# Performance work log

Measured on AMD Instinct MI355X. Metric: run time of the kernel, lower is better.

## Reference

```python
import jax, jax.numpy as jnp
import numpy as np

VOXEL_RES = 4
CLASSES = 40


def setup_inputs() -> dict:
    key = jax.random.key(0)
    kx, kw, kb = jax.random.split(key, 3)
    B, N = 64, 100000
    x = jax.random.normal(kx, (B, N, 3), dtype=jnp.float32)
    F = VOXEL_RES ** 3
    bound = 1.0 / np.sqrt(F)  # torch Linear default init range
    W = jax.random.uniform(kw, (CLASSES, F), minval=-bound, maxval=bound, dtype=jnp.float32)
    b = jax.random.uniform(kb, (CLASSES,), minval=-bound, maxval=bound, dtype=jnp.float32)
    return {"x": x, "W": W, "b": b}


def reference(x, W, b):
    # x: (B, N, 3). Faithful to torch.histogramdd(bins=R): the histogram range
    # per dimension is [min, max] of the data; the last bin is right-inclusive.
    B, N, _ = x.shape
    R = VOXEL_RES
    mn = jnp.min(x, axis=1, keepdims=True)  # (B, 1, 3)
    mx = jnp.max(x, axis=1, keepdims=True)  # (B, 1, 3)
    # bin index = floor((v - min) / (max - min) * R), clipped so v == max -> R-1
    idx = jnp.floor((x - mn) / (mx - mn) * R).astype(jnp.int32)
    idx = jnp.clip(idx, 0, R - 1)  # (B, N, 3)
    flat = idx[..., 0] * R * R + idx[..., 1] * R + idx[..., 2]  # (B, N)
    flat = flat + (jnp.arange(B, dtype=jnp.int32) * (R ** 3))[:, None]
    counts = jax.ops.segment_sum(
        jnp.ones((B * N,), dtype=x.dtype), flat.reshape(-1), num_segments=B * R ** 3
    ).reshape(B, R ** 3)
    counts = counts / N  # fraction of points per voxel
    class_outputs = counts @ W.T + b  # (B, classes)
    return class_outputs
```

## Files before the change

kernel.cpp:

```cpp
#include <hip/hip_runtime.h>

#define VR 4
#define NVOX 64
#define NCLS 40
#define NB 64
#define NPTS 100000
#define BPB 16
#define NBLK (NB * BPB)
#define G_PER_B (NPTS / 4)
#define F4_PER_B (NPTS * 3 / 4)
#define STRIDE_G (BPB * 256)
#define FULL_ITERS (G_PER_B / STRIDE_G)
#define TAIL_G (G_PER_B - FULL_ITERS * STRIDE_G)
#define SW_LD 41
#define FLT_BIG 3.402823466e38f

static __device__ __forceinline__ int bin1(float v, float mn, float s4) {
    int i = (int)((v - mn) * s4);
    return i > (VR - 1) ? (VR - 1) : i;
}

static __device__ __forceinline__ unsigned long long vox_mask(
        int v, const unsigned long long* ns) {
    return (__ballot(v & 1)  ^ ns[0]) & (__ballot(v & 2)  ^ ns[1])
         & (__ballot(v & 4)  ^ ns[2]) & (__ballot(v & 8)  ^ ns[3])
         & (__ballot(v & 16) ^ ns[4]) & (__ballot(v & 32) ^ ns[5]);
}


__global__ __launch_bounds__(256) void minmax_k(const float4* __restrict__ x,
                                                float* __restrict__ pmin,
                                                float* __restrict__ pmax,
                                                float* __restrict__ out) {
    const int bid = blockIdx.x;
    const int b = bid & (NB - 1);
    const int sub = bid >> 6;
    const float4* xb = x + (size_t)b * F4_PER_B;
    const int lane = threadIdx.x & 63;
    const int wv = threadIdx.x >> 6;
    const int t0 = sub * 256 + (int)threadIdx.x;

    if (sub == 0 && threadIdx.x < NCLS)
        out[b * NCLS + threadIdx.x] = 0.f;

    float mn0 = FLT_BIG, mn1 = FLT_BIG, mn2 = FLT_BIG;
    float mx0 = -FLT_BIG, mx1 = -FLT_BIG, mx2 = -FLT_BIG;
    #pragma unroll
    for (int k = 0; k < FULL_ITERS; k++) {
        const int g = t0 + k * STRIDE_G;
        const float4 a = xb[3 * g], c = xb[3 * g + 1], e = xb[3 * g + 2];
        mn0 = fminf(mn0, fminf(fminf(a.x, a.w), fminf(c.z, e.y)));
        mx0 = fmaxf(mx0, fmaxf(fmaxf(a.x, a.w), fmaxf(c.z, e.y)));
        mn1 = fminf(mn1, fminf(fminf(a.y, c.x), fminf(c.w, e.z)));
        mx1 = fmaxf(mx1, fmaxf(fmaxf(a.y, c.x), fmaxf(c.w, e.z)));
        mn2 = fminf(mn2, fminf(fminf(a.z, c.y), fminf(e.x, e.w)));
        mx2 = fmaxf(mx2, fmaxf(fmaxf(a.z, c.y), fmaxf(e.x, e.w)));
    }
    if (sub * 256 < TAIL_G && t0 < TAIL_G) {
        const int g = FULL_ITERS * STRIDE_G + t0;
        const float4 a = xb[3 * g], c = xb[3 * g + 1], e = xb[3 * g + 2];
        mn0 = fminf(mn0, fminf(fminf(a.x, a.w), fminf(c.z, e.y)));
        mx0 = fmaxf(mx0, fmaxf(fmaxf(a.x, a.w), fmaxf(c.z, e.y)));
        mn1 = fminf(mn1, fminf(fminf(a.y, c.x), fminf(c.w, e.z)));
        mx1 = fmaxf(mx1, fmaxf(fmaxf(a.y, c.x), fmaxf(c.w, e.z)));
        mn2 = fminf(mn2, fminf(fminf(a.z, c.y), fminf(e.x, e.w)));
        mx2 = fmaxf(mx2, fmaxf(fmaxf(a.z, c.y), fmaxf(e.x, e.w)));
    }

    #pragma unroll
    for (int off = 32; off > 0; off >>= 1) {
        mn0 = fminf(mn0, __shfl_down(mn0, off, 64));
        mn1 = fminf(mn1, __shfl_down(mn1, off, 64));
        mn2 = fminf(mn2, __shfl_down(mn2, off, 64));
        mx0 = fmaxf(mx0, __shfl_down(mx0, off, 64));
        mx1 = fmaxf(mx1, __shfl_down(mx1, off, 64));
        mx2 = fmaxf(mx2, __shfl_down(mx2, off, 64));
    }

    __shared__ float smn[4][3], smx[4][3];
    if (lane == 0) {
        smn[wv][0] = mn0; smn[wv][1] = mn1; smn[wv][2] = mn2;
        smx[wv][0] = mx0; smx[wv][1] = mx1; smx[wv][2] = mx2;
    }
    __syncthreads();
    if (threadIdx.x < 3) {
        const int d = threadIdx.x;
        float a = smn[0][d], z = smx[0][d];
        #pragma unroll
        for (int w = 1; w < 4; w++) {
            a = fminf(a, smn[w][d]);
            z = fmaxf(z, smx[w][d]);
        }
        pmin[(b * BPB + sub) * 3 + d] = a;
        pmax[(b * BPB + sub) * 3 + d] = z;
    }
}

__global__ __launch_bounds__(256) void hist_gemv_k(const float4* __restrict__ x,
                                                   const float* __restrict__ pmin,
                                                   const float* __restrict__ pmax,
                                                   const float* __restrict__ W,
                                                   const float* __restrict__ bias,
                                                   float* __restrict__ out) {
    const int bid = blockIdx.x;
    const int b = bid & (NB - 1);
    const int sub = bid >> 6;
    const float4* xb = x + (size_t)b * F4_PER_B;
    const int lane = threadIdx.x & 63;
    const int wv = threadIdx.x >> 6;
    const int t0 = sub * 256 + (int)threadIdx.x;

    __shared__ float sW[NVOX * SW_LD];
    __shared__ float smm[6];
    __shared__ unsigned swh[4][NVOX];
    __shared__ float fh[NVOX];

    for (int i = threadIdx.x; i < NCLS * NVOX; i += 256)
        sW[(i % NVOX) * SW_LD + (i / NVOX)] = W[i];

    if (threadIdx.x < 6) {
        const int d = threadIdx.x % 3;
        const bool isMax = threadIdx.x >= 3;
        float r = isMax ? -FLT_BIG : FLT_BIG;
        for (int s = 0; s < BPB; s++) {
            float v = isMax ? pmax[(b * BPB + s) * 3 + d]
                            : pmin[(b * BPB + s) * 3 + d];
            r = isMax ? fmaxf(r, v) : fminf(r, v);
        }
        smm[threadIdx.x] = r;
    }
    __syncthreads();
    const float bn0 = smm[0], bn1 = smm[1], bn2 = smm[2];
    const float s40 = (float)VR / (smm[3] - smm[0]);
    const float s41 = (float)VR / (smm[4] - smm[1]);
    const float s42 = (float)VR / (smm[5] - smm[2]);

    unsigned long long ns[6];
    #pragma unroll
    for (int k = 0; k < 6; k++)
        ns[k] = ((lane >> k) & 1) ? 0ull : ~0ull;

    unsigned cnt = 0;
    if (sub * 256 < TAIL_G) {
        const bool valid = t0 < TAIL_G;
        const unsigned long long vm = __ballot(valid);
        const int g = FULL_ITERS * STRIDE_G + (valid ? t0 : 0);
        const float4 a = xb[3 * g], c = xb[3 * g + 1], e = xb[3 * g + 2];
        int v0 = bin1(a.x, bn0, s40) * 16 + bin1(a.y, bn1, s41) * 4 + bin1(a.z, bn2, s42);
        int v1 = bin1(a.w, bn0, s40) * 16 + bin1(c.x, bn1, s41) * 4 + bin1(c.y, bn2, s42);
        int v2 = bin1(c.z, bn0, s40) * 16 + bin1(c.w, bn1, s41) * 4 + bin1(e.x, bn2, s42);
        int v3 = bin1(e.y, bn0, s40) * 16 + bin1(e.z, bn1, s41) * 4 + bin1(e.w, bn2, s42);
        cnt += (unsigned)__popcll(vm & vox_mask(v0, ns));
        cnt += (unsigned)__popcll(vm & vox_mask(v1, ns));
        cnt += (unsigned)__popcll(vm & vox_mask(v2, ns));
        cnt += (unsigned)__popcll(vm & vox_mask(v3, ns));
    }
    #pragma unroll 2
    for (int k = FULL_ITERS - 1; k >= 0; k--) {
        const int g = t0 + k * STRIDE_G;
        const float4 a = xb[3 * g], c = xb[3 * g + 1], e = xb[3 * g + 2];
        int v0 = bin1(a.x, bn0, s40) * 16 + bin1(a.y, bn1, s41) * 4 + bin1(a.z, bn2, s42);
        int v1 = bin1(a.w, bn0, s40) * 16 + bin1(c.x, bn1, s41) * 4 + bin1(c.y, bn2, s42);
        int v2 = bin1(c.z, bn0, s40) * 16 + bin1(c.w, bn1, s41) * 4 + bin1(e.x, bn2, s42);
        int v3 = bin1(e.y, bn0, s40) * 16 + bin1(e.z, bn1, s41) * 4 + bin1(e.w, bn2, s42);
        cnt += (unsigned)__popcll(vox_mask(v0, ns));
        cnt += (unsigned)__popcll(vox_mask(v1, ns));
        cnt += (unsigned)__popcll(vox_mask(v2, ns));
        cnt += (unsigned)__popcll(vox_mask(v3, ns));
    }

    swh[wv][lane] = cnt;
    __syncthreads();
    if (threadIdx.x < NVOX)
        fh[threadIdx.x] = (float)(swh[0][threadIdx.x] + swh[1][threadIdx.x] +
                                  swh[2][threadIdx.x] + swh[3][threadIdx.x])
                          * (1.0f / (float)NPTS);
    __syncthreads();
    if (threadIdx.x < NCLS) {
        const int c = threadIdx.x;
        float acc = (sub == 0) ? bias[c] : 0.f;
        #pragma unroll
        for (int f = 0; f < NVOX; f++)
            acc += fh[f] * sW[f * SW_LD + c];
        atomicAdd(&out[b * NCLS + c], acc);
    }
}

extern "C" void kernel_launch(void* const* d_in, const int* in_sizes, int n_in,
                              void* d_out, int out_size, void* d_ws, size_t ws_size,
                              hipStream_t stream) {
    const float4* x = (const float4*)d_in[0];
    const float* W = (const float*)d_in[1];
    const float* bias = (const float*)d_in[2];
    float* out = (float*)d_out;

    float* pmin = (float*)d_ws;
    float* pmax = pmin + NBLK * 3;

    minmax_k<<<NBLK, 256, 0, stream>>>(x, pmin, pmax, out);
    hist_gemv_k<<<NBLK, 256, 0, stream>>>(x, pmin, pmax, W, bias, out);
}
```

Baseline: 120.9 us.

## Use nontemporal loads for early minmax chunks and prefetch all histogram inputs

In minmax_k, the first NT_ITERS chunks of each batch are read with nontemporal loads so they do not push out cache lines, while the later chunks are read normally and can stay cached for the second pass. The second kernel loads all of its full-iteration data into registers up front, before the W staging and the min/max reduction. This overlaps the global-load latency with that setup work, and launch bounds raise the occupancy hint. The cost is much higher register pressure, since FULL_ITERS×3 float4 values are held per thread, which may cause spills or lower occupancy.

```diff
diff --git a/kernel.cpp b/kernel.cpp
--- a/kernel.cpp
+++ b/kernel.cpp
@@ -11,9 +11,12 @@
 #define F4_PER_B (NPTS * 3 / 4)
 #define STRIDE_G (BPB * 256)
 #define FULL_ITERS (G_PER_B / STRIDE_G)
+#define NT_ITERS 4
 #define TAIL_G (G_PER_B - FULL_ITERS * STRIDE_G)
 #define SW_LD 41
 #define FLT_BIG 3.402823466e38f
+
+typedef float f4 __attribute__((ext_vector_type(4)));
 
 static __device__ __forceinline__ int bin1(float v, float mn, float s4) {
     int i = (int)((v - mn) * s4);
@@ -28,14 +31,14 @@
 }
 
 
-__global__ __launch_bounds__(256) void minmax_k(const float4* __restrict__ x,
+__global__ __launch_bounds__(256) void minmax_k(const f4* __restrict__ x,
                                                 float* __restrict__ pmin,
                                                 float* __restrict__ pmax,
                                                 float* __restrict__ out) {
     const int bid = blockIdx.x;
     const int b = bid & (NB - 1);
     const int sub = bid >> 6;
-    const float4* xb = x + (size_t)b * F4_PER_B;
+    const f4* xb = x + (size_t)b * F4_PER_B;
     const int lane = threadIdx.x & 63;
     const int wv = threadIdx.x >> 6;
     const int t0 = sub * 256 + (int)threadIdx.x;
@@ -48,23 +51,30 @@
     #pragma unroll
     for (int k = 0; k < FULL_ITERS; k++) {
         const int g = t0 + k * STRIDE_G;
-        const float4 a = xb[3 * g], c = xb[3 * g + 1], e = xb[3 * g + 2];
-        mn0 = fminf(mn0, fminf(fminf(a.x, a.w), fminf(c.z, e.y)));
-        mx0 = fmaxf(mx0, fmaxf(fmaxf(a.x, a.w), fmaxf(c.z, e.y)));
-        mn1 = fminf(mn1, fminf(fminf(a.y, c.x), fminf(c.w, e.z)));
-        mx1 = fmaxf(mx1, fmaxf(fmaxf(a.y, c.x), fmaxf(c.w, e.z)));
-        mn2 = fminf(mn2, fminf(fminf(a.z, c.y), fminf(e.x, e.w)));
-        mx2 = fmaxf(mx2, fmaxf(fmaxf(a.z, c.y), fmaxf(e.x, e.w)));
+        f4 a, c, e;
+        if (k < NT_ITERS) {
+            a = __builtin_nontemporal_load(&xb[3 * g]);
+            c = __builtin_nontemporal_load(&xb[3 * g + 1]);
+            e = __builtin_nontemporal_load(&xb[3 * g + 2]);
+        } else {
+            a = xb[3 * g]; c = xb[3 * g + 1]; e = xb[3 * g + 2];
+        }
+        mn0 = fminf(mn0, fminf(fminf(a[0], a[3]), fminf(c[2], e[1])));
+        mx0 = fmaxf(mx0, fmaxf(fmaxf(a[0], a[3]), fmaxf(c[2], e[1])));
+        mn1 = fminf(mn1, fminf(fminf(a[1], c[0]), fminf(c[3], e[2])));
+        mx1 = fmaxf(mx1, fmaxf(fmaxf(a[1], c[0]), fmaxf(c[3], e[2])));
+        mn2 = fminf(mn2, fminf(fminf(a[2], c[1]), fminf(e[0], e[3])));
+        mx2 = fmaxf(mx2, fmaxf(fmaxf(a[2], c[1]), fmaxf(e[0], e[3])));
     }
     if (sub * 256 < TAIL_G && t0 < TAIL_G) {
         const int g = FULL_ITERS * STRIDE_G + t0;
-        const float4 a = xb[3 * g], c = xb[3 * g + 1], e = xb[3 * g + 2];
-        mn0 = fminf(mn0, fminf(fminf(a.x, a.w), fminf(c.z, e.y)));
-        mx0 = fmaxf(mx0, fmaxf(fmaxf(a.x, a.w), fmaxf(c.z, e.y)));
-        mn1 = fminf(mn1, fminf(fminf(a.y, c.x), fminf(c.w, e.z)));
-        mx1 = fmaxf(mx1, fmaxf(fmaxf(a.y, c.x), fmaxf(c.w, e.z)));
-        mn2 = fminf(mn2, fminf(fminf(a.z, c.y), fminf(e.x, e.w)));
-        mx2 = fmaxf(mx2, fmaxf(fmaxf(a.z, c.y), fmaxf(e.x, e.w)));
+        const f4 a = xb[3 * g], c = xb[3 * g + 1], e = xb[3 * g + 2];
+        mn0 = fminf(mn0, fminf(fminf(a[0], a[3]), fminf(c[2], e[1])));
+        mx0 = fmaxf(mx0, fmaxf(fmaxf(a[0], a[3]), fmaxf(c[2], e[1])));
+        mn1 = fminf(mn1, fminf(fminf(a[1], c[0]), fminf(c[3], e[2])));
+        mx1 = fmaxf(mx1, fmaxf(fmaxf(a[1], c[0]), fmaxf(c[3], e[2])));
+        mn2 = fminf(mn2, fminf(fminf(a[2], c[1]), fminf(e[0], e[3])));
+        mx2 = fmaxf(mx2, fmaxf(fmaxf(a[2], c[1]), fmaxf(e[0], e[3])));
     }
 
     #pragma unroll
@@ -96,16 +106,16 @@
     }
 }
 
-__global__ __launch_bounds__(256) void hist_gemv_k(const float4* __restrict__ x,
-                                                   const float* __restrict__ pmin,
-                                                   const float* __restrict__ pmax,
-                                                   const float* __restrict__ W,
-                                                   const float* __restrict__ bias,
-                                                   float* __restrict__ out) {
+__global__ __launch_bounds__(256, 4) void hist_gemv_k(const f4* __restrict__ x,
+                                                      const float* __restrict__ pmin,
+                                                      const float* __restrict__ pmax,
+                                                      const float* __restrict__ W,
+                                                      const float* __restrict__ bias,
+                                                      float* __restrict__ out) {
     const int bid = blockIdx.x;
     const int b = bid & (NB - 1);
     const int sub = bid >> 6;
-    const float4* xb = x + (size_t)b * F4_PER_B;
+    const f4* xb = x + (size_t)b * F4_PER_B;
     const int lane = threadIdx.x & 63;
     const int wv = threadIdx.x >> 6;
     const int t0 = sub * 256 + (int)threadIdx.x;
@@ -115,9 +125,15 @@
     __shared__ unsigned swh[4][NVOX];
     __shared__ float fh[NVOX];
 
+    f4 A[FULL_ITERS], C[FULL_ITERS], E[FULL_ITERS];
+    #pragma unroll
+    for (int k = FULL_ITERS - 1; k >= 0; k--) {
+        const int g = t0 + k * STRIDE_G;
+        A[k] = xb[3 * g]; C[k] = xb[3 * g + 1]; E[k] = xb[3 * g + 2];
+    }
+
     for (int i = threadIdx.x; i < NCLS * NVOX; i += 256)
         sW[(i % NVOX) * SW_LD + (i / NVOX)] = W[i];
-
     if (threadIdx.x < 6) {
         const int d = threadIdx.x % 3;
         const bool isMax = threadIdx.x >= 3;
@@ -145,24 +161,23 @@
         const bool valid = t0 < TAIL_G;
         const unsigned long long vm = __ballot(valid);
         const int g = FULL_ITERS * STRIDE_G + (valid ? t0 : 0);
-        const float4 a = xb[3 * g], c = xb[3 * g + 1], e = xb[3 * g + 2];
-        int v0 = bin1(a.x, bn0, s40) * 16 + bin1(a.y, bn1, s41) * 4 + bin1(a.z, bn2, s42);
-        int v1 = bin1(a.w, bn0, s40) * 16 + bin1(c.x, bn1, s41) * 4 + bin1(c.y, bn2, s42);
-        int v2 = bin1(c.z, bn0, s40) * 16 + bin1(c.w, bn1, s41) * 4 + bin1(e.x, bn2, s42);
-        int v3 = bin1(e.y, bn0, s40) * 16 + bin1(e.z, bn1, s41) * 4 + bin1(e.w, bn2, s42);
+        const f4 a = xb[3 * g], c = xb[3 * g + 1], e = xb[3 * g + 2];
+        int v0 = bin1(a[0], bn0, s40) * 16 + bin1(a[1], bn1, s41) * 4 + bin1(a[2], bn2, s42);
+        int v1 = bin1(a[3], bn0, s40) * 16 + bin1(c[0], bn1, s41) * 4 + bin1(c[1], bn2, s42);
+        int v2 = bin1(c[2], bn0, s40) * 16 + bin1(c[3], bn1, s41) * 4 + bin1(e[0], bn2, s42);
+        int v3 = bin1(e[1], bn0, s40) * 16 + bin1(e[2], bn1, s41) * 4 + bin1(e[3], bn2, s42);
         cnt += (unsigned)__popcll(vm & vox_mask(v0, ns));
         cnt += (unsigned)__popcll(vm & vox_mask(v1, ns));
         cnt += (unsigned)__popcll(vm & vox_mask(v2, ns));
         cnt += (unsigned)__popcll(vm & vox_mask(v3, ns));
     }
-    #pragma unroll 2
+    #pragma unroll
     for (int k = FULL_ITERS - 1; k >= 0; k--) {
-        const int g = t0 + k * STRIDE_G;
-        const float4 a = xb[3 * g], c = xb[3 * g + 1], e = xb[3 * g + 2];
-        int v0 = bin1(a.x, bn0, s40) * 16 + bin1(a.y, bn1, s41) * 4 + bin1(a.z, bn2, s42);
-        int v1 = bin1(a.w, bn0, s40) * 16 + bin1(c.x, bn1, s41) * 4 + bin1(c.y, bn2, s42);
-        int v2 = bin1(c.z, bn0, s40) * 16 + bin1(c.w, bn1, s41) * 4 + bin1(e.x, bn2, s42);
-        int v3 = bin1(e.y, bn0, s40) * 16 + bin1(e.z, bn1, s41) * 4 + bin1(e.w, bn2, s42);
+        const f4 a = A[k], c = C[k], e = E[k];
+        int v0 = bin1(a[0], bn0, s40) * 16 + bin1(a[1], bn1, s41) * 4 + bin1(a[2], bn2, s42);
+        int v1 = bin1(a[3], bn0, s40) * 16 + bin1(c[0], bn1, s41) * 4 + bin1(c[1], bn2, s42);
+        int v2 = bin1(c[2], bn0, s40) * 16 + bin1(c[3], bn1, s41) * 4 + bin1(e[0], bn2, s42);
+        int v3 = bin1(e[1], bn0, s40) * 16 + bin1(e[2], bn1, s41) * 4 + bin1(e[3], bn2, s42);
         cnt += (unsigned)__popcll(vox_mask(v0, ns));
         cnt += (unsigned)__popcll(vox_mask(v1, ns));
         cnt += (unsigned)__popcll(vox_mask(v2, ns));
@@ -189,7 +204,7 @@
 extern "C" void kernel_launch(void* const* d_in, const int* in_sizes, int n_in,
                               void* d_out, int out_size, void* d_ws, size_t ws_size,
                               hipStream_t stream) {
-    const float4* x = (const float4*)d_in[0];
+    const f4* x = (const f4*)d_in[0];
     const float* W = (const float*)d_in[1];
     const float* bias = (const float*)d_in[2];
     float* out = (float*)d_out;
```

Result: slower. 128.1 us (+5.9%).
